# Kernel tuning notes

Measured on AMD Instinct MI355X. Metric: run time of the kernel, lower is better.

The kernel has to match this reference:

```python
import jax, jax.numpy as jnp
import numpy as np

N_NODES = 50000
N_EDGES = 800000
D_IN = 128
D_HID = 128
D_OUT = 128


def gcn_conv(x, W, b, src, dst, n_nodes):
    """PyG GCNConv: sym-normalized A+I aggregation, then bias.
    messages flow src -> dst; self-loops handled analytically."""
    h = x @ W  # [N, F_out]
    ones = jnp.ones(src.shape[0], dtype=h.dtype)
    deg = jax.ops.segment_sum(ones, dst, num_segments=n_nodes) + 1.0  # +1 self-loop
    dinv = jax.lax.rsqrt(deg)  # deg^-1/2
    norm = dinv[src] * dinv[dst]  # [E]
    agg = jax.ops.segment_sum(h[src] * norm[:, None], dst, num_segments=n_nodes)
    out = agg + h * (dinv * dinv)[:, None]  # self-loop term: dinv[i]^2 * h[i]
    return out + b


def setup_inputs() -> dict:
    key = jax.random.key(0)
    ks = jax.random.split(key, 12)
    x = jax.random.normal(ks[0], (N_NODES, D_IN), dtype=jnp.float32)
    edge_index = jax.random.randint(ks[1], (2, N_EDGES), 0, N_NODES, dtype=jnp.int64)

    def lin(k, fi, fo):
        s = 1.0 / np.sqrt(fi)
        return jax.random.uniform(k, (fi, fo), jnp.float32, -s, s)

    return {
        "x": x,
        "edge_index": edge_index,
        "W1": lin(ks[2], D_IN, D_HID), "b1": jnp.zeros((D_HID,), jnp.float32),
        "W2": lin(ks[3], D_HID, D_HID), "b2": jnp.zeros((D_HID,), jnp.float32),
        "W3": lin(ks[4], D_HID, D_OUT), "b3": jnp.zeros((D_OUT,), jnp.float32),
        "Wm1": lin(ks[5], 2 * D_HID, D_HID), "bm1": jnp.zeros((D_HID,), jnp.float32),
        "Wm2": lin(ks[6], D_HID, D_HID), "bm2": jnp.zeros((D_HID,), jnp.float32),
    }


def reference(x, edge_index, W1, b1, W2, b2, W3, b3, Wm1, bm1, Wm2, bm2):
    src, dst = edge_index[0], edge_index[1]
    n = x.shape[0]
    h = jax.nn.relu(gcn_conv(x, W1, b1, src, dst, n))
    h = jax.nn.relu(gcn_conv(h, W2, b2, src, dst, n))
    h = gcn_conv(h, W3, b3, src, dst, n)
    # edge head: gather node pairs, concat, 2-layer MLP
    ef = jnp.concatenate([h[src], h[dst]], axis=1)  # [E, 2*hidden]
    es = jax.nn.relu(ef @ Wm1 + bm1) @ Wm2 + bm2  # [E, hidden]
    return jnp.squeeze(es)
```

## Files before the change

kernel.cpp:

```cpp
#include <hip/hip_runtime.h>
#include <stdint.h>

typedef __attribute__((ext_vector_type(8))) short bf16x8;
typedef __attribute__((ext_vector_type(4))) float f32x4;

static __device__ __forceinline__ unsigned short f2b(float f) {
    unsigned int u = __float_as_uint(f);
    unsigned int r = u + 0x7fffu + ((u >> 16) & 1u);
    return (unsigned short)(r >> 16);
}
static __device__ __forceinline__ float b2f(unsigned short u) {
    return __uint_as_float((unsigned int)u << 16);
}
static __device__ __forceinline__ f32x4 b2f4(ushort4 u) {
    f32x4 r;
    r[0] = b2f(u.x); r[1] = b2f(u.y); r[2] = b2f(u.z); r[3] = b2f(u.w);
    return r;
}


__global__ void count_deg(const int* __restrict__ dst, int E, int* __restrict__ counts) {
    int e = blockIdx.x * 256 + threadIdx.x;
    if (e < E) atomicAdd(&counts[dst[e]], 1);
}

__global__ void scan_s1(const int* __restrict__ counts, int N,
                        int* __restrict__ rowstart, float* __restrict__ dinv,
                        int* __restrict__ psum) {
    __shared__ int wsum[16];
    int tid = threadIdx.x, wave = tid >> 6, lane = tid & 63;
    int i = blockIdx.x * 1024 + tid;
    int c = (i < N) ? counts[i] : 0;
    int x = c;
    #pragma unroll
    for (int off = 1; off < 64; off <<= 1) {
        int v = __shfl_up(x, off);
        if (lane >= off) x += v;
    }
    if (lane == 63) wsum[wave] = x;
    __syncthreads();
    int pre = 0, tot = 0;
    #pragma unroll
    for (int w = 0; w < 16; ++w) {
        int s = wsum[w];
        tot += s;
        if (w < wave) pre += s;
    }
    if (i < N) {
        rowstart[i] = pre + x - c;
        dinv[i] = rsqrtf((float)c + 1.0f);
    }
    if (tid == 0) psum[blockIdx.x] = tot;
}

__global__ void scan_s2(int* __restrict__ psum, int nchunk,
                        int* __restrict__ rowstart, int N) {
    __shared__ int wsum[16];
    int tid = threadIdx.x, wave = tid >> 6, lane = tid & 63;
    int v = (tid < nchunk) ? psum[tid] : 0;
    int x = v;
    #pragma unroll
    for (int off = 1; off < 64; off <<= 1) {
        int s = __shfl_up(x, off);
        if (lane >= off) x += s;
    }
    if (lane == 63) wsum[wave] = x;
    __syncthreads();
    int pre = 0, tot = 0;
    #pragma unroll
    for (int w = 0; w < 16; ++w) {
        int s = wsum[w];
        tot += s;
        if (w < wave) pre += s;
    }
    if (tid < nchunk) psum[tid] = pre + x - v;
    if (tid == 0) rowstart[N] = tot;
}

__global__ void scan_s3(int* __restrict__ rowstart, const int* __restrict__ psum,
                        int N, int* __restrict__ cursor) {
    int i = blockIdx.x * 1024 + threadIdx.x;
    if (i < N) {
        int r = rowstart[i] + psum[blockIdx.x];
        rowstart[i] = r;
        cursor[i] = r;
    }
}

__global__ void fill_csr(const int* __restrict__ src, const int* __restrict__ dst, int E,
                         int* __restrict__ cursor, int* __restrict__ csr_src) {
    int e = blockIdx.x * 256 + threadIdx.x;
    if (e < E) {
        int p = atomicAdd(&cursor[dst[e]], 1);
        csr_src[p] = src[e];
    }
}


__global__ __launch_bounds__(256) void node_gemm(const float* __restrict__ in,
                                                 const float* __restrict__ W,
                                                 unsigned short* __restrict__ outb, int N) {
    __shared__ __align__(16) float rl[64][128];
    int tid = threadIdx.x;
    int rowbase = blockIdx.x * 64;
    #pragma unroll
    for (int p = 0; p < 8; ++p) {
        int idx = p * 256 + tid;
        int r = idx >> 5, c4 = (idx & 31) * 4;
        int row = rowbase + r;
        if (row >= N) row = N - 1;
        *(float4*)&rl[r][c4] = *(const float4*)(in + (size_t)row * 128 + c4);
    }
    __syncthreads();
    int rg = tid >> 5, cg = tid & 31, f0 = cg * 4;
    f32x4 acc[8];
    #pragma unroll
    for (int i = 0; i < 8; ++i) acc[i] = (f32x4){0.f, 0.f, 0.f, 0.f};
    for (int k = 0; k < 128; k += 4) {
        f32x4 w0 = *(const f32x4*)&W[(k + 0) * 128 + f0];
        f32x4 w1 = *(const f32x4*)&W[(k + 1) * 128 + f0];
        f32x4 w2 = *(const f32x4*)&W[(k + 2) * 128 + f0];
        f32x4 w3 = *(const f32x4*)&W[(k + 3) * 128 + f0];
        #pragma unroll
        for (int i = 0; i < 8; ++i) {
            f32x4 r4 = *(const f32x4*)&rl[rg * 8 + i][k];
            acc[i] += r4[0] * w0;
            acc[i] += r4[1] * w1;
            acc[i] += r4[2] * w2;
            acc[i] += r4[3] * w3;
        }
    }
    #pragma unroll
    for (int i = 0; i < 8; ++i) {
        int row = rowbase + rg * 8 + i;
        if (row < N) {
            unsigned int u0 = (unsigned int)f2b(acc[i][0]) | ((unsigned int)f2b(acc[i][1]) << 16);
            unsigned int u1 = (unsigned int)f2b(acc[i][2]) | ((unsigned int)f2b(acc[i][3]) << 16);
            *(uint2*)(outb + (size_t)row * 128 + f0) = make_uint2(u0, u1);
        }
    }
}


template <int RELU, int BF16OUT>
__global__ __launch_bounds__(256) void aggregate(
        const unsigned short* __restrict__ tb, const int* __restrict__ rowstart,
        const int* __restrict__ csr_src, const float* __restrict__ dinv,
        const float* __restrict__ bias, float* __restrict__ hout,
        unsigned short* __restrict__ hb_out, int N) {
    int tid = threadIdx.x;
    int node = blockIdx.x * 8 + (tid >> 5);
    if (node >= N) return;
    int c = (tid & 31) * 4;
    float di = dinv[node];
    f32x4 self = b2f4(*(const ushort4*)(tb + (size_t)node * 128 + c));
    f32x4 acc = *(const f32x4*)(bias + c) + (di * di) * self;
    int rs = rowstart[node], re = rowstart[node + 1];
    int e = rs;
    for (; e + 1 < re; e += 2) {
        int s0 = csr_src[e], s1 = csr_src[e + 1];
        float n0 = dinv[s0] * di;
        float n1 = dinv[s1] * di;
        f32x4 t0 = b2f4(*(const ushort4*)(tb + (size_t)s0 * 128 + c));
        f32x4 t1 = b2f4(*(const ushort4*)(tb + (size_t)s1 * 128 + c));
        acc += n0 * t0;
        acc += n1 * t1;
    }
    if (e < re) {
        int s0 = csr_src[e];
        acc += (dinv[s0] * di) * b2f4(*(const ushort4*)(tb + (size_t)s0 * 128 + c));
    }
    if (RELU) {
        #pragma unroll
        for (int j = 0; j < 4; ++j) acc[j] = fmaxf(acc[j], 0.f);
    }
    if (BF16OUT) {
        unsigned int u0 = (unsigned int)f2b(acc[0]) | ((unsigned int)f2b(acc[1]) << 16);
        unsigned int u1 = (unsigned int)f2b(acc[2]) | ((unsigned int)f2b(acc[3]) << 16);
        *(uint2*)(hb_out + (size_t)node * 128 + c) = make_uint2(u0, u1);
    } else {
        *(f32x4*)(hout + (size_t)node * 128 + c) = acc;
    }
}


__global__ __launch_bounds__(256) void uv_gemm(const unsigned short* __restrict__ h3b,
                                               const float* __restrict__ Wm1,
                                               unsigned short* __restrict__ uvb, int N) {
    __shared__ __align__(16) unsigned short hl[64][136];
    int tid = threadIdx.x;
    int wid = tid >> 6, lane = tid & 63;
    int lg = lane >> 4, l15 = lane & 15;
    int tilebase = blockIdx.x * 64;

    bf16x8 a[4][4];
    #pragma unroll
    for (int mt = 0; mt < 4; ++mt) {
        int jc = wid * 64 + mt * 16 + l15;
        int koff = (jc >> 7) * 128;
        int col = jc & 127;
        #pragma unroll
        for (int kk = 0; kk < 4; ++kk) {
            bf16x8 af;
            #pragma unroll
            for (int ee = 0; ee < 8; ++ee)
                af[ee] = (short)f2b(Wm1[(size_t)(koff + kk * 32 + lg * 8 + ee) * 128 + col]);
            a[mt][kk] = af;
        }
    }

    #pragma unroll
    for (int p = 0; p < 4; ++p) {
        int idx = p * 256 + tid;
        int r = idx >> 4, ci = idx & 15;
        int row = tilebase + r;
        if (row >= N) row = N - 1;
        uint4 v = *(const uint4*)(h3b + (size_t)row * 128 + ci * 8);
        *(uint4*)&hl[r][ci * 8] = v;
    }
    __syncthreads();

    f32x4 acc[4][4];
    #pragma unroll
    for (int mt = 0; mt < 4; ++mt)
        #pragma unroll
        for (int nt = 0; nt < 4; ++nt) acc[mt][nt] = (f32x4){0.f, 0.f, 0.f, 0.f};
    #pragma unroll
    for (int kk = 0; kk < 4; ++kk) {
        #pragma unroll
        for (int nt = 0; nt < 4; ++nt) {
            bf16x8 b = *(const bf16x8*)&hl[nt * 16 + l15][kk * 32 + lg * 8];
            #pragma unroll
            for (int mt = 0; mt < 4; ++mt)
                acc[mt][nt] = __builtin_amdgcn_mfma_f32_16x16x32_bf16(a[mt][kk], b, acc[mt][nt], 0, 0, 0);
        }
    }
    #pragma unroll
    for (int mt = 0; mt < 4; ++mt) {
        int jc = wid * 64 + mt * 16 + lg * 4;
        #pragma unroll
        for (int nt = 0; nt < 4; ++nt) {
            int node = tilebase + nt * 16 + l15;
            if (node < N) {
                unsigned int u0 = (unsigned int)f2b(acc[mt][nt][0]) | ((unsigned int)f2b(acc[mt][nt][1]) << 16);
                unsigned int u1 = (unsigned int)f2b(acc[mt][nt][2]) | ((unsigned int)f2b(acc[mt][nt][3]) << 16);
                *(uint2*)(uvb + (size_t)node * 256 + jc) = make_uint2(u0, u1);
            }
        }
    }
}


__global__ __launch_bounds__(256, 3) void edge_head2(
        const unsigned short* __restrict__ uvb, const int* __restrict__ src,
        const int* __restrict__ dst, const float* __restrict__ bm1,
        const float* __restrict__ Wm2, const float* __restrict__ bm2,
        float* __restrict__ out, int E, int ntiles) {
    __shared__ __align__(16) unsigned short zl[64][136];
    int tid = threadIdx.x;
    int wid = tid >> 6, lane = tid & 63;
    int lg = lane >> 4, l15 = lane & 15;
    int es = tid >> 4;
    int ci = tid & 15;
    int c0 = ci * 8;

    bf16x8 a2[2][4];
    float b2v[2][4];
    #pragma unroll
    for (int mt = 0; mt < 2; ++mt) {
        int m = wid * 32 + mt * 16 + l15;
        #pragma unroll
        for (int kk = 0; kk < 4; ++kk) {
            bf16x8 af;
            #pragma unroll
            for (int ee = 0; ee < 8; ++ee)
                af[ee] = (short)f2b(Wm2[(size_t)(kk * 32 + lg * 8 + ee) * 128 + m]);
            a2[mt][kk] = af;
        }
        #pragma unroll
        for (int r = 0; r < 4; ++r)
            b2v[mt][r] = bm2[wid * 32 + mt * 16 + lg * 4 + r];
    }
    float bm1v[8];
    #pragma unroll
    for (int j = 0; j < 8; ++j) bm1v[j] = bm1[c0 + j];

    for (int tile = blockIdx.x; tile < ntiles; tile += gridDim.x) {
        __syncthreads();
        #pragma unroll
        for (int p = 0; p < 4; ++p) {
            int eg = tile * 64 + p * 16 + es;
            if (eg >= E) eg = E - 1;
            int s = src[eg], d = dst[eg];
            uint4 uu = *(const uint4*)(uvb + (size_t)s * 256 + c0);
            uint4 vv = *(const uint4*)(uvb + (size_t)d * 256 + 128 + c0);
            unsigned int w[4];
            {
                float z0 = fmaxf(b2f((unsigned short)(uu.x)) + b2f((unsigned short)(vv.x)) + bm1v[0], 0.f);
                float z1 = fmaxf(b2f((unsigned short)(uu.x >> 16)) + b2f((unsigned short)(vv.x >> 16)) + bm1v[1], 0.f);
                float z2 = fmaxf(b2f((unsigned short)(uu.y)) + b2f((unsigned short)(vv.y)) + bm1v[2], 0.f);
                float z3 = fmaxf(b2f((unsigned short)(uu.y >> 16)) + b2f((unsigned short)(vv.y >> 16)) + bm1v[3], 0.f);
                float z4 = fmaxf(b2f((unsigned short)(uu.z)) + b2f((unsigned short)(vv.z)) + bm1v[4], 0.f);
                float z5 = fmaxf(b2f((unsigned short)(uu.z >> 16)) + b2f((unsigned short)(vv.z >> 16)) + bm1v[5], 0.f);
                float z6 = fmaxf(b2f((unsigned short)(uu.w)) + b2f((unsigned short)(vv.w)) + bm1v[6], 0.f);
                float z7 = fmaxf(b2f((unsigned short)(uu.w >> 16)) + b2f((unsigned short)(vv.w >> 16)) + bm1v[7], 0.f);
                w[0] = (unsigned int)f2b(z0) | ((unsigned int)f2b(z1) << 16);
                w[1] = (unsigned int)f2b(z2) | ((unsigned int)f2b(z3) << 16);
                w[2] = (unsigned int)f2b(z4) | ((unsigned int)f2b(z5) << 16);
                w[3] = (unsigned int)f2b(z6) | ((unsigned int)f2b(z7) << 16);
            }
            *(uint4*)&zl[p * 16 + es][c0] = make_uint4(w[0], w[1], w[2], w[3]);
        }
        __syncthreads();

        f32x4 c2[2][4];
        #pragma unroll
        for (int mt = 0; mt < 2; ++mt)
            #pragma unroll
            for (int nt = 0; nt < 4; ++nt) c2[mt][nt] = (f32x4){0.f, 0.f, 0.f, 0.f};
        #pragma unroll
        for (int kk = 0; kk < 4; ++kk) {
            #pragma unroll
            for (int nt = 0; nt < 4; ++nt) {
                bf16x8 b = *(const bf16x8*)&zl[nt * 16 + l15][kk * 32 + lg * 8];
                c2[0][nt] = __builtin_amdgcn_mfma_f32_16x16x32_bf16(a2[0][kk], b, c2[0][nt], 0, 0, 0);
                c2[1][nt] = __builtin_amdgcn_mfma_f32_16x16x32_bf16(a2[1][kk], b, c2[1][nt], 0, 0, 0);
            }
        }
        #pragma unroll
        for (int mt = 0; mt < 2; ++mt) {
            #pragma unroll
            for (int nt = 0; nt < 4; ++nt) {
                int eg = tile * 64 + nt * 16 + l15;
                if (eg < E) {
                    f32x4 o;
                    #pragma unroll
                    for (int r = 0; r < 4; ++r) o[r] = c2[mt][nt][r] + b2v[mt][r];
                    *(f32x4*)(out + (size_t)eg * 128 + wid * 32 + mt * 16 + lg * 4) = o;
                }
            }
        }
    }
}


extern "C" void kernel_launch(void* const* d_in, const int* in_sizes, int n_in,
                              void* d_out, int out_size, void* d_ws, size_t ws_size,
                              hipStream_t stream) {
    const float* x  = (const float*)d_in[0];
    const int*   ei = (const int*)d_in[1];
    const float* W1 = (const float*)d_in[2];
    const float* b1 = (const float*)d_in[3];
    const float* W2 = (const float*)d_in[4];
    const float* b2 = (const float*)d_in[5];
    const float* W3 = (const float*)d_in[6];
    const float* b3 = (const float*)d_in[7];
    const float* Wm1 = (const float*)d_in[8];
    const float* bm1 = (const float*)d_in[9];
    const float* Wm2 = (const float*)d_in[10];
    const float* bm2 = (const float*)d_in[11];
    float* out = (float*)d_out;

    const int N = in_sizes[0] / 128;
    const int E = in_sizes[1] / 2;
    const int* src = ei;
    const int* dstp = ei + E;

    uintptr_t base = (uintptr_t)d_ws;
    auto alloc = [&](size_t bytes) -> void* {
        uintptr_t p = base;
        base += (bytes + 255) & ~(uintptr_t)255;
        return (void*)p;
    };
    int*   counts   = (int*)alloc((size_t)(N + 1) * 4);
    int*   rowstart = (int*)alloc((size_t)(N + 1) * 4);
    int*   cursor   = (int*)alloc((size_t)N * 4);
    float* dinv     = (float*)alloc((size_t)N * 4);
    int*   psum     = (int*)alloc(4096);
    int*   csr      = (int*)alloc((size_t)E * 4);
    unsigned short* tb  = (unsigned short*)alloc((size_t)N * 128 * 2);
    float* h        = (float*)alloc((size_t)N * 128 * 4);
    unsigned short* h3b = (unsigned short*)alloc((size_t)N * 128 * 2);
    unsigned short* uvb = (unsigned short*)alloc((size_t)N * 256 * 2);
    (void)ws_size; (void)n_in; (void)out_size;

    hipMemsetAsync(counts, 0, (size_t)(N + 1) * 4, stream);

    int egrid = (E + 255) / 256;
    int nchunk = (N + 1023) / 1024;
    count_deg<<<egrid, 256, 0, stream>>>(dstp, E, counts);
    scan_s1<<<nchunk, 1024, 0, stream>>>(counts, N, rowstart, dinv, psum);
    scan_s2<<<1, 1024, 0, stream>>>(psum, nchunk, rowstart, N);
    scan_s3<<<nchunk, 1024, 0, stream>>>(rowstart, psum, N, cursor);
    fill_csr<<<egrid, 256, 0, stream>>>(src, dstp, E, cursor, csr);

    int ggrid = (N + 63) / 64;
    int agrid = (N + 7) / 8;
    node_gemm<<<ggrid, 256, 0, stream>>>(x, W1, tb, N);
    aggregate<1, 0><<<agrid, 256, 0, stream>>>(tb, rowstart, csr, dinv, b1, h, nullptr, N);
    node_gemm<<<ggrid, 256, 0, stream>>>(h, W2, tb, N);
    aggregate<1, 0><<<agrid, 256, 0, stream>>>(tb, rowstart, csr, dinv, b2, h, nullptr, N);
    node_gemm<<<ggrid, 256, 0, stream>>>(h, W3, tb, N);
    aggregate<0, 1><<<agrid, 256, 0, stream>>>(tb, rowstart, csr, dinv, b3, nullptr, h3b, N);

    uv_gemm<<<ggrid, 256, 0, stream>>>(h3b, Wm1, uvb, N);

    int ntiles = (E + 63) / 64;
    int hgrid = ntiles < 1024 ? ntiles : 1024;
    edge_head2<<<hgrid, 256, 0, stream>>>(uvb, src, dstp, bm1, Wm2, bm2, out, E, ntiles);
}
```

Baseline: 501.8 us.

## Use MFMA node GEMMs, bf16 hidden activations, and CSR-ordered edge head

Measured after the change: 464.1 us. -7.5%, faster.

```diff
diff --git a/kernel.cpp b/kernel.cpp
--- a/kernel.cpp
+++ b/kernel.cpp
@@ -88,66 +88,101 @@
 }
 
 __global__ void fill_csr(const int* __restrict__ src, const int* __restrict__ dst, int E,
-                         int* __restrict__ cursor, int* __restrict__ csr_src) {
+                         int* __restrict__ cursor, int* __restrict__ csr_src,
+                         int* __restrict__ csr_dst, int* __restrict__ csr_eid) {
     int e = blockIdx.x * 256 + threadIdx.x;
     if (e < E) {
-        int p = atomicAdd(&cursor[dst[e]], 1);
+        int d = dst[e];
+        int p = atomicAdd(&cursor[d], 1);
         csr_src[p] = src[e];
-    }
-}
-
-
-__global__ __launch_bounds__(256) void node_gemm(const float* __restrict__ in,
+        csr_dst[p] = d;
+        csr_eid[p] = e;
+    }
+}
+
+
+template <int IN_F32>
+__global__ __launch_bounds__(256) void node_mfma(const void* __restrict__ inp,
                                                  const float* __restrict__ W,
                                                  unsigned short* __restrict__ outb, int N) {
-    __shared__ __align__(16) float rl[64][128];
+    __shared__ __align__(16) unsigned short hl[64][136];
     int tid = threadIdx.x;
-    int rowbase = blockIdx.x * 64;
-    #pragma unroll
-    for (int p = 0; p < 8; ++p) {
+    int wid = tid >> 6, lane = tid & 63;
+    int lg = lane >> 4, l15 = lane & 15;
+    int tilebase = blockIdx.x * 64;
+
+    bf16x8 a[2][4];
+    #pragma unroll
+    for (int mt = 0; mt < 2; ++mt) {
+        int col = wid * 32 + mt * 16 + l15;
+        #pragma unroll
+        for (int kk = 0; kk < 4; ++kk) {
+            bf16x8 af;
+            #pragma unroll
+            for (int ee = 0; ee < 8; ++ee)
+                af[ee] = (short)f2b(W[(size_t)(kk * 32 + lg * 8 + ee) * 128 + col]);
+            a[mt][kk] = af;
+        }
+    }
+
+    #pragma unroll
+    for (int p = 0; p < 4; ++p) {
         int idx = p * 256 + tid;
-        int r = idx >> 5, c4 = (idx & 31) * 4;
-        int row = rowbase + r;
+        int r = idx >> 4, ci = idx & 15;
+        int row = tilebase + r;
         if (row >= N) row = N - 1;
-        *(float4*)&rl[r][c4] = *(const float4*)(in + (size_t)row * 128 + c4);
+        if (IN_F32) {
+            const float* ip = (const float*)inp + (size_t)row * 128 + ci * 8;
+            f32x4 x0 = *(const f32x4*)ip;
+            f32x4 x1 = *(const f32x4*)(ip + 4);
+            uint4 v;
+            v.x = (unsigned int)f2b(x0[0]) | ((unsigned int)f2b(x0[1]) << 16);
+            v.y = (unsigned int)f2b(x0[2]) | ((unsigned int)f2b(x0[3]) << 16);
+            v.z = (unsigned int)f2b(x1[0]) | ((unsigned int)f2b(x1[1]) << 16);
+            v.w = (unsigned int)f2b(x1[2]) | ((unsigned int)f2b(x1[3]) << 16);
+            *(uint4*)&hl[r][ci * 8] = v;
+        } else {
+            *(uint4*)&hl[r][ci * 8] =
+                *(const uint4*)((const unsigned short*)inp + (size_t)row * 128 + ci * 8);
+        }
     }
     __syncthreads();
-    int rg = tid >> 5, cg = tid & 31, f0 = cg * 4;
-    f32x4 acc[8];
-    #pragma unroll
-    for (int i = 0; i < 8; ++i) acc[i] = (f32x4){0.f, 0.f, 0.f, 0.f};
-    for (int k = 0; k < 128; k += 4) {
-        f32x4 w0 = *(const f32x4*)&W[(k + 0) * 128 + f0];
-        f32x4 w1 = *(const f32x4*)&W[(k + 1) * 128 + f0];
-        f32x4 w2 = *(const f32x4*)&W[(k + 2) * 128 + f0];
-        f32x4 w3 = *(const f32x4*)&W[(k + 3) * 128 + f0];
-        #pragma unroll
-        for (int i = 0; i < 8; ++i) {
-            f32x4 r4 = *(const f32x4*)&rl[rg * 8 + i][k];
-            acc[i] += r4[0] * w0;
-            acc[i] += r4[1] * w1;
-            acc[i] += r4[2] * w2;
-            acc[i] += r4[3] * w3;
-        }
-    }
-    #pragma unroll
-    for (int i = 0; i < 8; ++i) {
-        int row = rowbase + rg * 8 + i;
-        if (row < N) {
-            unsigned int u0 = (unsigned int)f2b(acc[i][0]) | ((unsigned int)f2b(acc[i][1]) << 16);
-            unsigned int u1 = (unsigned int)f2b(acc[i][2]) | ((unsigned int)f2b(acc[i][3]) << 16);
-            *(uint2*)(outb + (size_t)row * 128 + f0) = make_uint2(u0, u1);
-        }
-    }
-}
-
-
-template <int RELU, int BF16OUT>
+
+    f32x4 acc[2][4];
+    #pragma unroll
+    for (int mt = 0; mt < 2; ++mt)
+        #pragma unroll
+        for (int nt = 0; nt < 4; ++nt) acc[mt][nt] = (f32x4){0.f, 0.f, 0.f, 0.f};
+    #pragma unroll
+    for (int kk = 0; kk < 4; ++kk) {
+        #pragma unroll
+        for (int nt = 0; nt < 4; ++nt) {
+            bf16x8 b = *(const bf16x8*)&hl[nt * 16 + l15][kk * 32 + lg * 8];
+            acc[0][nt] = __builtin_amdgcn_mfma_f32_16x16x32_bf16(a[0][kk], b, acc[0][nt], 0, 0, 0);
+            acc[1][nt] = __builtin_amdgcn_mfma_f32_16x16x32_bf16(a[1][kk], b, acc[1][nt], 0, 0, 0);
+        }
+    }
+    #pragma unroll
+    for (int mt = 0; mt < 2; ++mt) {
+        int j = wid * 32 + mt * 16 + lg * 4;
+        #pragma unroll
+        for (int nt = 0; nt < 4; ++nt) {
+            int node = tilebase + nt * 16 + l15;
+            if (node < N) {
+                unsigned int u0 = (unsigned int)f2b(acc[mt][nt][0]) | ((unsigned int)f2b(acc[mt][nt][1]) << 16);
+                unsigned int u1 = (unsigned int)f2b(acc[mt][nt][2]) | ((unsigned int)f2b(acc[mt][nt][3]) << 16);
+                *(uint2*)(outb + (size_t)node * 128 + j) = make_uint2(u0, u1);
+            }
+        }
+    }
+}
+
+
+template <int RELU>
 __global__ __launch_bounds__(256) void aggregate(
         const unsigned short* __restrict__ tb, const int* __restrict__ rowstart,
         const int* __restrict__ csr_src, const float* __restrict__ dinv,
-        const float* __restrict__ bias, float* __restrict__ hout,
-        unsigned short* __restrict__ hb_out, int N) {
+        const float* __restrict__ bias, unsigned short* __restrict__ hb, int N) {
     int tid = threadIdx.x;
     int node = blockIdx.x * 8 + (tid >> 5);
     if (node >= N) return;
@@ -174,13 +209,9 @@
         #pragma unroll
         for (int j = 0; j < 4; ++j) acc[j] = fmaxf(acc[j], 0.f);
     }
-    if (BF16OUT) {
-        unsigned int u0 = (unsigned int)f2b(acc[0]) | ((unsigned int)f2b(acc[1]) << 16);
-        unsigned int u1 = (unsigned int)f2b(acc[2]) | ((unsigned int)f2b(acc[3]) << 16);
-        *(uint2*)(hb_out + (size_t)node * 128 + c) = make_uint2(u0, u1);
-    } else {
-        *(f32x4*)(hout + (size_t)node * 128 + c) = acc;
-    }
+    unsigned int u0 = (unsigned int)f2b(acc[0]) | ((unsigned int)f2b(acc[1]) << 16);
+    unsigned int u1 = (unsigned int)f2b(acc[2]) | ((unsigned int)f2b(acc[3]) << 16);
+    *(uint2*)(hb + (size_t)node * 128 + c) = make_uint2(u0, u1);
 }
 
 
@@ -251,12 +282,13 @@
 }
 
 
-__global__ __launch_bounds__(256, 3) void edge_head2(
-        const unsigned short* __restrict__ uvb, const int* __restrict__ src,
-        const int* __restrict__ dst, const float* __restrict__ bm1,
-        const float* __restrict__ Wm2, const float* __restrict__ bm2,
-        float* __restrict__ out, int E, int ntiles) {
+__global__ __launch_bounds__(256, 3) void edge_head3(
+        const unsigned short* __restrict__ uvb, const int* __restrict__ csr_src,
+        const int* __restrict__ csr_dst, const int* __restrict__ csr_eid,
+        const float* __restrict__ bm1, const float* __restrict__ Wm2,
+        const float* __restrict__ bm2, float* __restrict__ out, int E, int ntiles) {
     __shared__ __align__(16) unsigned short zl[64][136];
+    __shared__ int eid_l[64];
     int tid = threadIdx.x;
     int wid = tid >> 6, lane = tid & 63;
     int lg = lane >> 4, l15 = lane & 15;
@@ -289,9 +321,10 @@
         __syncthreads();
         #pragma unroll
         for (int p = 0; p < 4; ++p) {
-            int eg = tile * 64 + p * 16 + es;
-            if (eg >= E) eg = E - 1;
-            int s = src[eg], d = dst[eg];
+            int slot = tile * 64 + p * 16 + es;
+            int cs = (slot < E) ? slot : (E - 1);
+            int s = csr_src[cs], d = csr_dst[cs];
+            if (ci == 0) eid_l[p * 16 + es] = (slot < E) ? csr_eid[cs] : -1;
             uint4 uu = *(const uint4*)(uvb + (size_t)s * 256 + c0);
             uint4 vv = *(const uint4*)(uvb + (size_t)d * 256 + 128 + c0);
             unsigned int w[4];
@@ -331,8 +364,8 @@
         for (int mt = 0; mt < 2; ++mt) {
             #pragma unroll
             for (int nt = 0; nt < 4; ++nt) {
-                int eg = tile * 64 + nt * 16 + l15;
-                if (eg < E) {
+                int eg = eid_l[nt * 16 + l15];
+                if (eg >= 0) {
                     f32x4 o;
                     #pragma unroll
                     for (int r = 0; r < 4; ++r) o[r] = c2[mt][nt][r] + b2v[mt][r];
@@ -377,10 +410,11 @@
     int*   cursor   = (int*)alloc((size_t)N * 4);
     float* dinv     = (float*)alloc((size_t)N * 4);
     int*   psum     = (int*)alloc(4096);
-    int*   csr      = (int*)alloc((size_t)E * 4);
+    int*   csr_s    = (int*)alloc((size_t)E * 4);
+    int*   csr_d    = (int*)alloc((size_t)E * 4);
+    int*   csr_e    = (int*)alloc((size_t)E * 4);
     unsigned short* tb  = (unsigned short*)alloc((size_t)N * 128 * 2);
-    float* h        = (float*)alloc((size_t)N * 128 * 4);
-    unsigned short* h3b = (unsigned short*)alloc((size_t)N * 128 * 2);
+    unsigned short* hb  = (unsigned short*)alloc((size_t)N * 128 * 2);
     unsigned short* uvb = (unsigned short*)alloc((size_t)N * 256 * 2);
     (void)ws_size; (void)n_in; (void)out_size;
 
@@ -392,20 +426,20 @@
     scan_s1<<<nchunk, 1024, 0, stream>>>(counts, N, rowstart, dinv, psum);
     scan_s2<<<1, 1024, 0, stream>>>(psum, nchunk, rowstart, N);
     scan_s3<<<nchunk, 1024, 0, stream>>>(rowstart, psum, N, cursor);
-    fill_csr<<<egrid, 256, 0, stream>>>(src, dstp, E, cursor, csr);
+    fill_csr<<<egrid, 256, 0, stream>>>(src, dstp, E, cursor, csr_s, csr_d, csr_e);
 
     int ggrid = (N + 63) / 64;
     int agrid = (N + 7) / 8;
-    node_gemm<<<ggrid, 256, 0, stream>>>(x, W1, tb, N);
-    aggregate<1, 0><<<agrid, 256, 0, stream>>>(tb, rowstart, csr, dinv, b1, h, nullptr, N);
-    node_gemm<<<ggrid, 256, 0, stream>>>(h, W2, tb, N);
-    aggregate<1, 0><<<agrid, 256, 0, stream>>>(tb, rowstart, csr, dinv, b2, h, nullptr, N);
-    node_gemm<<<ggrid, 256, 0, stream>>>(h, W3, tb, N);
-    aggregate<0, 1><<<agrid, 256, 0, stream>>>(tb, rowstart, csr, dinv, b3, nullptr, h3b, N);
-
-    uv_gemm<<<ggrid, 256, 0, stream>>>(h3b, Wm1, uvb, N);
+    node_mfma<1><<<ggrid, 256, 0, stream>>>(x, W1, tb, N);
+    aggregate<1><<<agrid, 256, 0, stream>>>(tb, rowstart, csr_s, dinv, b1, hb, N);
+    node_mfma<0><<<ggrid, 256, 0, stream>>>(hb, W2, tb, N);
+    aggregate<1><<<agrid, 256, 0, stream>>>(tb, rowstart, csr_s, dinv, b2, hb, N);
+    node_mfma<0><<<ggrid, 256, 0, stream>>>(hb, W3, tb, N);
+    aggregate<0><<<agrid, 256, 0, stream>>>(tb, rowstart, csr_s, dinv, b3, hb, N);
+
+    uv_gemm<<<ggrid, 256, 0, stream>>>(hb, Wm1, uvb, N);
 
     int ntiles = (E + 63) / 64;
     int hgrid = ntiles < 1024 ? ntiles : 1024;
-    edge_head2<<<hgrid, 256, 0, stream>>>(uvb, src, dstp, bm1, Wm2, bm2, out, E, ntiles);
-}
+    edge_head3<<<hgrid, 256, 0, stream>>>(uvb, csr_s, csr_d, csr_e, bm1, Wm2, bm2, out, E, ntiles);
+}
```
